# Performance work log

Hardware: AMD Instinct MI355X
Metric: run time of the kernel (lower is better)

The kernel has to match this reference:

```python
import jax, jax.numpy as jnp
import numpy as np
from jax import lax

IN_CH = 512
OUT_CH = 512
K = 3
W_DIM = 512
PAD = K // 2
EPS = 1e-8


def setup_inputs() -> dict:
    key = jax.random.key(0)
    k1, k2, k3, k4 = jax.random.split(key, 4)
    B, H, W = 8, 64, 64
    x = jax.random.normal(k1, (B, IN_CH, H, W), dtype=jnp.float32)
    w = jax.random.normal(k2, (B, W_DIM), dtype=jnp.float32)
    weight = jax.random.normal(k3, (OUT_CH, IN_CH, K, K), dtype=jnp.float32)
    bias = jnp.zeros((OUT_CH,), dtype=jnp.float32)
    # nn.Linear(512, in_ch): weight [in_ch, 512], bias [in_ch]
    lim = 1.0 / np.sqrt(W_DIM)
    affine_w = jax.random.uniform(k4, (IN_CH, W_DIM), dtype=jnp.float32, minval=-lim, maxval=lim)
    affine_b = jnp.zeros((IN_CH,), dtype=jnp.float32)
    return {"x": x, "w": w, "weight": weight, "bias": bias,
            "affine_w": affine_w, "affine_b": affine_b}


def _conv_one(xi, wi):
    # xi: [C, H, W], wi: [O, C, K, K] -> [O, H, W]
    out = lax.conv_general_dilated(
        xi[None], wi, window_strides=(1, 1),
        padding=[(PAD, PAD), (PAD, PAD)],
        dimension_numbers=("NCHW", "OIHW", "NCHW"))
    return out[0]


def reference(x, w, weight, bias, affine_w, affine_b):
    # style: [B, C] -> broadcast as [B, 1, C, 1, 1]
    style = w @ affine_w.T + affine_b
    wmod = weight[None] * (style[:, None, :, None, None] + 1.0)  # [B, O, C, K, K]
    # demodulate
    sigma = lax.rsqrt(jnp.sum(wmod * wmod, axis=(2, 3, 4), keepdims=True) + EPS)
    wmod = wmod * sigma
    # per-sample conv (equivalent to groups=B grouped conv)
    out = jax.vmap(_conv_one)(x, wmod)  # [B, O, H, W]
    return out + bias[None, :, None, None]
```

## Files before the change

kernel.cpp:

```cpp
#include <hip/hip_runtime.h>
#include <hip/hip_bf16.h>

typedef __attribute__((ext_vector_type(8))) short bf16x8;
typedef __attribute__((ext_vector_type(4))) float f32x4;

#define FSW(c) (((c) >> 1) & 3)

static __device__ __forceinline__ uint bf16rne(float f) {
    uint u = __float_as_uint(f);
    return (u + 0x7fffu + ((u >> 16) & 1u)) >> 16;
}

__global__ void k_prep1(const float* __restrict__ weight, ushort* __restrict__ Wf,
                        float* __restrict__ wsq, const float* __restrict__ w,
                        const float* __restrict__ aw, const float* __restrict__ ab,
                        float* __restrict__ style) {
    if (blockIdx.x < 1024) {
        int t = blockIdx.x * 256 + threadIdx.x;
        int o = t >> 9, c = t & 511;
        int grp = o >> 5, rr = o & 31, fm = rr >> 4, l15r = rr & 15;
        int chunkid = c >> 5, kgw = (c >> 3) & 3, kk = c & 7;
        int lanew = kgw * 16 + l15r;
        const float* wp = weight + (size_t)t * 9;
        size_t G = (size_t)(grp * 16 + chunkid);
        size_t base = G * 9216 + (size_t)fm * 512 + (size_t)lanew * 8 + kk;
        float sq = 0.f;
        #pragma unroll
        for (int j = 0; j < 9; ++j) {
            float v = wp[j];
            sq += v * v;
            Wf[base + (size_t)j * 1024] = (ushort)bf16rne(v);
        }
        wsq[t] = sq;
    } else {
        int idx = (blockIdx.x - 1024) * 4 + (threadIdx.x >> 6);
        int lane = threadIdx.x & 63;
        int b = idx >> 9, c = idx & 511;
        const float* wp = w + b * 512;
        const float* ap = aw + (size_t)c * 512;
        float s = 0.f;
        #pragma unroll
        for (int i = 0; i < 8; ++i) s += wp[lane + i * 64] * ap[lane + i * 64];
        #pragma unroll
        for (int m = 32; m; m >>= 1) s += __shfl_xor(s, m, 64);
        if (lane == 0) style[idx] = s + ab[c] + 1.0f;
    }
}

__global__ void k_prep2(const float* __restrict__ style, const float* __restrict__ wsq,
                        float* __restrict__ sigma, const float* __restrict__ x,
                        ushort* __restrict__ xb) {
    if (blockIdx.x < 1024) {
        int idx = blockIdx.x * 4 + (threadIdx.x >> 6);
        int lane = threadIdx.x & 63;
        int b = idx >> 9, o = idx & 511;
        const float* sp = style + b * 512;
        const float* qp = wsq + (size_t)o * 512;
        float s = 0.f;
        #pragma unroll
        for (int i = 0; i < 8; ++i) {
            float st = sp[lane + i * 64];
            s += st * st * qp[lane + i * 64];
        }
        #pragma unroll
        for (int m = 32; m; m >>= 1) s += __shfl_xor(s, m, 64);
        if (lane == 0) sigma[idx] = rsqrtf(s + 1e-8f);
    } else {
        int bid = blockIdx.x - 1024;
        int b = bid >> 6, y = bid & 63;
        int xcol = threadIdx.x >> 2, cg = threadIdx.x & 3;
        const float* sp = style + b * 512;
        #pragma unroll 1
        for (int cb = 0; cb < 16; ++cb) {
            int c0 = cb * 32 + cg * 8;
            float v[8];
            #pragma unroll
            for (int j = 0; j < 8; ++j)
                v[j] = x[((size_t)(b * 512 + c0 + j) * 64 + y) * 64 + xcol] * sp[c0 + j];
            uint4 pk;
            pk.x = bf16rne(v[0]) | (bf16rne(v[1]) << 16);
            pk.y = bf16rne(v[2]) | (bf16rne(v[3]) << 16);
            pk.z = bf16rne(v[4]) | (bf16rne(v[5]) << 16);
            pk.w = bf16rne(v[6]) | (bf16rne(v[7]) << 16);
            *(uint4*)&xb[((size_t)(b * 64 + y) * 64 + xcol) * 512 + c0] = pk;
        }
    }
}

#define ALOAD(SL, DY, CC) { \
    const ushort* p_ = Wbase + (size_t)(CC) * 9216 + (DY) * 3072; \
    _Pragma("unroll") for (int q_ = 0; q_ < 6; ++q_) \
        SL[q_] = *(const uint4*)(p_ + q_ * 512); }

#define MM(AV, BV, FM, FN) \
    acc[FM][FN] = __builtin_amdgcn_mfma_f32_16x16x32_bf16( \
        *(const bf16x8*)&(AV), (BV), acc[FM][FN], 0, 0, 0)

#define HGROUP(AARR, H) \
    _Pragma("unroll") for (int dx_ = 0; dx_ < 3; ++dx_) { \
      _Pragma("unroll") for (int q_ = 0; q_ < 4; ++q_) { \
        MM(AARR[dx_ * 2 + 0], bv[dx_ * 4 + q_], 0, (H) * 4 + q_); \
        MM(AARR[dx_ * 2 + 1], bv[dx_ * 4 + q_], 1, (H) * 4 + q_); \
      } }

#define ROW(R, MFMAS) { \
    bf16x8 bv[12]; \
    _Pragma("unroll") for (int dx_ = 0; dx_ < 3; ++dx_) \
    _Pragma("unroll") for (int q_ = 0; q_ < 4; ++q_) { \
        int ci_ = dx_ + q_ * 16 + l15; \
        bv[dx_ * 4 + q_] = *(const bf16x8*)&sX[cur][((R) * 66 + ci_) * 32 + ((kg ^ FSW(ci_)) * 8)]; \
    } \
    __builtin_amdgcn_s_setprio(1); \
    MFMAS \
    __builtin_amdgcn_s_setprio(0); }

__global__ __launch_bounds__(256, 2) void k_conv(
    const ushort* __restrict__ xb, const ushort* __restrict__ Wf,
    const float* __restrict__ sigma, const float* __restrict__ bias,
    float* __restrict__ out) {

    __shared__ ushort sX[2][4 * 66 * 32];

    const int tid = threadIdx.x, bid = blockIdx.x;
    const int ob = bid >> 8;
    const int pb = ((bid & 7) << 5) | ((bid >> 3) & 31);
    const int b = pb >> 5, y0 = (pb & 31) * 2;
    const int o0 = ob * 128;
    const int wv = tid >> 6, lane = tid & 63;
    const int l15 = lane & 15, kg = lane >> 4;

    const int scol = (tid >> 2) & 63;
    const int skg = tid & 3;
    const int colpos = scol + 1;
    const int sslot = (skg ^ FSW(colpos)) * 8;
    const ushort* xrow_base = xb + ((size_t)(b * 64) * 64 + scol) * 512 + skg * 8;

    const int grp = ob * 4 + wv;
    const ushort* Wbase = Wf + (size_t)grp * 147456 + lane * 8;

    f32x4 acc[2][8];
    #pragma unroll
    for (int i = 0; i < 2; ++i)
        #pragma unroll
        for (int j = 0; j < 8; ++j) acc[i][j] = (f32x4){0.f, 0.f, 0.f, 0.f};

    if (tid < 64) {
        int buf = tid >> 5, rem = tid & 31;
        int r = rem >> 3, side = (rem >> 2) & 1, sl = rem & 3;
        int cp = side * 65;
        *(uint4*)&sX[buf][(r * 66 + cp) * 32 + sl * 8] = make_uint4(0u, 0u, 0u, 0u);
    }

    uint4 xs[4];
    #pragma unroll
    for (int p = 0; p < 4; ++p) {
        int yy = y0 - 1 + p;
        xs[p] = ((unsigned)yy < 64u)
              ? *(const uint4*)(xrow_base + (size_t)yy * 32768)
              : make_uint4(0u, 0u, 0u, 0u);
    }
    #pragma unroll
    for (int p = 0; p < 4; ++p)
        *(uint4*)&sX[0][(p * 66 + colpos) * 32 + sslot] = xs[p];

    uint4 a0[6], a1[6], a2[6];
    ALOAD(a0, 0, 0) ALOAD(a1, 1, 0) ALOAD(a2, 2, 0)
    __syncthreads();

    int cur = 0;
    #pragma unroll 1
    for (int cci = 0; cci < 16; ++cci) {
        const int ncc = (cci + 1) & 15;

        #pragma unroll
        for (int p = 0; p < 4; ++p) {
            int yy = y0 - 1 + p;
            xs[p] = ((unsigned)yy < 64u)
                  ? *(const uint4*)(xrow_base + (size_t)yy * 32768 + ncc * 32)
                  : make_uint4(0u, 0u, 0u, 0u);
        }

        ROW(0, HGROUP(a0, 0))
        ROW(1, HGROUP(a0, 1) HGROUP(a1, 0))
        ALOAD(a0, 0, ncc)
        ROW(2, HGROUP(a1, 1) HGROUP(a2, 0))
        ALOAD(a1, 1, ncc)
        ROW(3, HGROUP(a2, 1))

        #pragma unroll
        for (int p = 0; p < 4; ++p)
            *(uint4*)&sX[cur ^ 1][(p * 66 + colpos) * 32 + sslot] = xs[p];
        __syncthreads();
        cur ^= 1;
        ALOAD(a2, 2, ncc)
    }

    const float* sigb = sigma + b * 512;
    #pragma unroll
    for (int fm = 0; fm < 2; ++fm) {
        #pragma unroll
        for (int j = 0; j < 4; ++j) {
            int o = o0 + wv * 32 + fm * 16 + kg * 4 + j;
            float sg = sigb[o];
            float bs = bias[o];
            float* op = out + ((size_t)(b * 512 + o) * 64 + y0) * 64;
            #pragma unroll
            for (int fn = 0; fn < 8; ++fn)
                op[(fn >> 2) * 64 + (fn & 3) * 16 + l15] = acc[fm][fn][j] * sg + bs;
        }
    }
}

extern "C" void kernel_launch(void* const* d_in, const int* in_sizes, int n_in,
                              void* d_out, int out_size, void* d_ws, size_t ws_size,
                              hipStream_t stream) {
    const float* x    = (const float*)d_in[0];
    const float* w    = (const float*)d_in[1];
    const float* wt   = (const float*)d_in[2];
    const float* bias = (const float*)d_in[3];
    const float* aw   = (const float*)d_in[4];
    const float* ab   = (const float*)d_in[5];
    float* out = (float*)d_out;

    float* style  = (float*)d_ws;
    float* sigmap = style + 4096;
    float* wsq    = sigmap + 4096;
    ushort* Wf    = (ushort*)(wsq + 512 * 512);
    ushort* xbm   = Wf + 2359296;

    k_prep1<<<2048, 256, 0, stream>>>(wt, Wf, wsq, w, aw, ab, style);
    k_prep2<<<1536, 256, 0, stream>>>(style, wsq, sigmap, x, xbm);
    k_conv <<<1024, 256, 0, stream>>>(xbm, Wf, sigmap, bias, out);
}
```

Before: 142.4 us.

## Process two channel chunks per barrier using four LDS planes, drop setprio

The conv main loop now handles two 32-channel chunks per iteration and stages input tiles in four LDS planes (two pairs) instead of two. This halves the number of __syncthreads barriers per block and keeps the weight register prefetch pipelined across both halves. The s_setprio hints around the MFMA groups are also removed. In exchange LDS use per block doubles (about 67 KB), which could limit occupancy to fewer than the two blocks per CU requested.

```diff
diff --git a/kernel.cpp b/kernel.cpp
--- a/kernel.cpp
+++ b/kernel.cpp
@@ -103,23 +103,33 @@
         MM(AARR[dx_ * 2 + 1], bv[dx_ * 4 + q_], 1, (H) * 4 + q_); \
       } }
 
-#define ROW(R, MFMAS) { \
+#define ROW(PL, R, MFMAS) { \
     bf16x8 bv[12]; \
     _Pragma("unroll") for (int dx_ = 0; dx_ < 3; ++dx_) \
     _Pragma("unroll") for (int q_ = 0; q_ < 4; ++q_) { \
         int ci_ = dx_ + q_ * 16 + l15; \
-        bv[dx_ * 4 + q_] = *(const bf16x8*)&sX[cur][((R) * 66 + ci_) * 32 + ((kg ^ FSW(ci_)) * 8)]; \
+        bv[dx_ * 4 + q_] = *(const bf16x8*)&(PL)[((R) * 66 + ci_) * 32 + ((kg ^ FSW(ci_)) * 8)]; \
     } \
-    __builtin_amdgcn_s_setprio(1); \
-    MFMAS \
-    __builtin_amdgcn_s_setprio(0); }
+    MFMAS }
+
+#define XLOAD(CC) { \
+    _Pragma("unroll") for (int p_ = 0; p_ < 4; ++p_) { \
+        int yy_ = y0 - 1 + p_; \
+        xs[p_] = ((unsigned)yy_ < 64u) \
+               ? *(const uint4*)(xrow_base + (size_t)yy_ * 32768 + (CC) * 32) \
+               : make_uint4(0u, 0u, 0u, 0u); \
+    } }
+
+#define XWRITE(PL) { \
+    _Pragma("unroll") for (int p_ = 0; p_ < 4; ++p_) \
+        *(uint4*)&(PL)[(p_ * 66 + colpos) * 32 + sslot] = xs[p_]; }
 
 __global__ __launch_bounds__(256, 2) void k_conv(
     const ushort* __restrict__ xb, const ushort* __restrict__ Wf,
     const float* __restrict__ sigma, const float* __restrict__ bias,
     float* __restrict__ out) {
 
-    __shared__ ushort sX[2][4 * 66 * 32];
+    __shared__ ushort sX[4][4 * 66 * 32];
 
     const int tid = threadIdx.x, bid = blockIdx.x;
     const int ob = bid >> 8;
@@ -144,24 +154,16 @@
         #pragma unroll
         for (int j = 0; j < 8; ++j) acc[i][j] = (f32x4){0.f, 0.f, 0.f, 0.f};
 
-    if (tid < 64) {
-        int buf = tid >> 5, rem = tid & 31;
+    if (tid < 128) {
+        int pl = tid >> 5, rem = tid & 31;
         int r = rem >> 3, side = (rem >> 2) & 1, sl = rem & 3;
         int cp = side * 65;
-        *(uint4*)&sX[buf][(r * 66 + cp) * 32 + sl * 8] = make_uint4(0u, 0u, 0u, 0u);
+        *(uint4*)&sX[pl][(r * 66 + cp) * 32 + sl * 8] = make_uint4(0u, 0u, 0u, 0u);
     }
 
     uint4 xs[4];
-    #pragma unroll
-    for (int p = 0; p < 4; ++p) {
-        int yy = y0 - 1 + p;
-        xs[p] = ((unsigned)yy < 64u)
-              ? *(const uint4*)(xrow_base + (size_t)yy * 32768)
-              : make_uint4(0u, 0u, 0u, 0u);
-    }
-    #pragma unroll
-    for (int p = 0; p < 4; ++p)
-        *(uint4*)&sX[0][(p * 66 + colpos) * 32 + sslot] = xs[p];
+    XLOAD(0) XWRITE(sX[0])
+    XLOAD(1) XWRITE(sX[1])
 
     uint4 a0[6], a1[6], a2[6];
     ALOAD(a0, 0, 0) ALOAD(a1, 1, 0) ALOAD(a2, 2, 0)
@@ -169,30 +171,33 @@
 
     int cur = 0;
     #pragma unroll 1
-    for (int cci = 0; cci < 16; ++cci) {
-        const int ncc = (cci + 1) & 15;
-
-        #pragma unroll
-        for (int p = 0; p < 4; ++p) {
-            int yy = y0 - 1 + p;
-            xs[p] = ((unsigned)yy < 64u)
-                  ? *(const uint4*)(xrow_base + (size_t)yy * 32768 + ncc * 32)
-                  : make_uint4(0u, 0u, 0u, 0u);
-        }
-
-        ROW(0, HGROUP(a0, 0))
-        ROW(1, HGROUP(a0, 1) HGROUP(a1, 0))
-        ALOAD(a0, 0, ncc)
-        ROW(2, HGROUP(a1, 1) HGROUP(a2, 0))
-        ALOAD(a1, 1, ncc)
-        ROW(3, HGROUP(a2, 1))
-
-        #pragma unroll
-        for (int p = 0; p < 4; ++p)
-            *(uint4*)&sX[cur ^ 1][(p * 66 + colpos) * 32 + sslot] = xs[p];
+    for (int it = 0; it < 8; ++it) {
+        const int c1 = it * 2 + 1;
+        const int n0 = (it * 2 + 2) & 15, n1 = (it * 2 + 3) & 15;
+        const int cur2 = cur * 2;
+
+        XLOAD(n0)
+        ROW(sX[cur2], 0, HGROUP(a0, 0))
+        ROW(sX[cur2], 1, HGROUP(a0, 1) HGROUP(a1, 0))
+        ALOAD(a0, 0, c1)
+        ROW(sX[cur2], 2, HGROUP(a1, 1) HGROUP(a2, 0))
+        ALOAD(a1, 1, c1)
+        ROW(sX[cur2], 3, HGROUP(a2, 1))
+        XWRITE(sX[cur2 ^ 2])
+
+        XLOAD(n1)
+        ALOAD(a2, 2, c1)
+        ROW(sX[cur2 + 1], 0, HGROUP(a0, 0))
+        ROW(sX[cur2 + 1], 1, HGROUP(a0, 1) HGROUP(a1, 0))
+        ALOAD(a0, 0, n0)
+        ROW(sX[cur2 + 1], 2, HGROUP(a1, 1) HGROUP(a2, 0))
+        ALOAD(a1, 1, n0)
+        ROW(sX[cur2 + 1], 3, HGROUP(a2, 1))
+        XWRITE(sX[(cur2 ^ 2) + 1])
+
         __syncthreads();
         cur ^= 1;
-        ALOAD(a2, 2, ncc)
+        ALOAD(a2, 2, n0)
     }
 
     const float* sigb = sigma + b * 512;
```

Measured after the change: 147.9 us. 1.04x slower.

## Retile conv waves to 2x2 layout with 64 out-channels by 32 columns

Applied to the files above, without the earlier changes.

Changes each wave's output tile from 32 out-channels by 64 pixels to 64 out-channels by 32 pixels, arranged as a 2x2 wave grid. Each wave now reads half as many shared-memory B fragments per row and twice as many A (weight) fragments from global memory. The A-register pipeline is reworked to ping-pong two 12-entry buffers across chunk pairs, with the loop unrolled by two. The aim is less LDS traffic per MFMA, at the cost of duplicated global weight loads across wave pairs and higher register pressure.

```diff
diff --git a/kernel.cpp b/kernel.cpp
--- a/kernel.cpp
+++ b/kernel.cpp
@@ -88,31 +88,55 @@
 }
 
 #define ALOAD(SL, DY, CC) { \
-    const ushort* p_ = Wbase + (size_t)(CC) * 9216 + (DY) * 3072; \
-    _Pragma("unroll") for (int q_ = 0; q_ < 6; ++q_) \
-        SL[q_] = *(const uint4*)(p_ + q_ * 512); }
-
-#define MM(AV, BV, FM, FN) \
-    acc[FM][FN] = __builtin_amdgcn_mfma_f32_16x16x32_bf16( \
-        *(const bf16x8*)&(AV), (BV), acc[FM][FN], 0, 0, 0)
+    _Pragma("unroll") for (int dx_ = 0; dx_ < 3; ++dx_) \
+    _Pragma("unroll") for (int fm_ = 0; fm_ < 4; ++fm_) \
+        SL[dx_ * 4 + fm_] = *(const uint4*)((fm_ < 2 ? Wbase0 : Wbase1) \
+            + (size_t)(CC) * 9216 + ((DY) * 3 + dx_) * 1024 + (fm_ & 1) * 512); }
 
 #define HGROUP(AARR, H) \
-    _Pragma("unroll") for (int dx_ = 0; dx_ < 3; ++dx_) { \
-      _Pragma("unroll") for (int q_ = 0; q_ < 4; ++q_) { \
-        MM(AARR[dx_ * 2 + 0], bv[dx_ * 4 + q_], 0, (H) * 4 + q_); \
-        MM(AARR[dx_ * 2 + 1], bv[dx_ * 4 + q_], 1, (H) * 4 + q_); \
-      } }
+    _Pragma("unroll") for (int dx_ = 0; dx_ < 3; ++dx_) \
+    _Pragma("unroll") for (int q_ = 0; q_ < 2; ++q_) \
+    _Pragma("unroll") for (int fm_ = 0; fm_ < 4; ++fm_) \
+        acc[fm_][(H) * 2 + q_] = __builtin_amdgcn_mfma_f32_16x16x32_bf16( \
+            *(const bf16x8*)&AARR[dx_ * 4 + fm_], bv[dx_ * 2 + q_], \
+            acc[fm_][(H) * 2 + q_], 0, 0, 0);
 
 #define ROW(R, MFMAS) { \
-    bf16x8 bv[12]; \
+    bf16x8 bv[6]; \
     _Pragma("unroll") for (int dx_ = 0; dx_ < 3; ++dx_) \
-    _Pragma("unroll") for (int q_ = 0; q_ < 4; ++q_) { \
-        int ci_ = dx_ + q_ * 16 + l15; \
-        bv[dx_ * 4 + q_] = *(const bf16x8*)&sX[cur][((R) * 66 + ci_) * 32 + ((kg ^ FSW(ci_)) * 8)]; \
+    _Pragma("unroll") for (int q_ = 0; q_ < 2; ++q_) { \
+        int ci_ = dx_ + cb32 + q_ * 16 + l15; \
+        bv[dx_ * 2 + q_] = *(const bf16x8*)&sX[cur][((R) * 66 + ci_) * 32 + ((kg ^ FSW(ci_)) * 8)]; \
     } \
     __builtin_amdgcn_s_setprio(1); \
     MFMAS \
     __builtin_amdgcn_s_setprio(0); }
+
+#define XLOAD(CC) { \
+    _Pragma("unroll") for (int p_ = 0; p_ < 4; ++p_) { \
+        int yy_ = y0 - 1 + p_; \
+        xs[p_] = ((unsigned)yy_ < 64u) \
+               ? *(const uint4*)(xrow_base + (size_t)yy_ * 32768 + (CC) * 32) \
+               : make_uint4(0u, 0u, 0u, 0u); \
+    } }
+
+#define XWRITE(BUF) { \
+    _Pragma("unroll") for (int p_ = 0; p_ < 4; ++p_) \
+        *(uint4*)&sX[BUF][(p_ * 66 + colpos) * 32 + sslot] = xs[p_]; }
+
+#define CHUNK(CCI, NCC, A0_, A1_) { \
+    XLOAD(NCC) \
+    ROW(0, HGROUP(A0_, 0)) \
+    ROW(1, HGROUP(A0_, 1) HGROUP(A1_, 0)) \
+    ALOAD(A0_, 2, CCI)             \
+    ROW(2, HGROUP(A1_, 1) HGROUP(A0_, 0)) \
+    ALOAD(A1_, 0, NCC)             \
+    ROW(3, HGROUP(A0_, 1)) \
+    XWRITE(cur ^ 1) \
+    __syncthreads(); \
+    cur ^= 1; \
+    ALOAD(A0_, 1, NCC)             \
+}
 
 __global__ __launch_bounds__(256, 2) void k_conv(
     const ushort* __restrict__ xb, const ushort* __restrict__ Wf,
@@ -128,6 +152,8 @@
     const int o0 = ob * 128;
     const int wv = tid >> 6, lane = tid & 63;
     const int l15 = lane & 15, kg = lane >> 4;
+    const int wr = wv >> 1;
+    const int cb32 = (wv & 1) * 32;
 
     const int scol = (tid >> 2) & 63;
     const int skg = tid & 3;
@@ -135,14 +161,14 @@
     const int sslot = (skg ^ FSW(colpos)) * 8;
     const ushort* xrow_base = xb + ((size_t)(b * 64) * 64 + scol) * 512 + skg * 8;
 
-    const int grp = ob * 4 + wv;
-    const ushort* Wbase = Wf + (size_t)grp * 147456 + lane * 8;
-
-    f32x4 acc[2][8];
+    const ushort* Wbase0 = Wf + (size_t)(ob * 4 + wr * 2) * 147456 + lane * 8;
+    const ushort* Wbase1 = Wbase0 + 147456;
+
+    f32x4 acc[4][4];
     #pragma unroll
-    for (int i = 0; i < 2; ++i)
-        #pragma unroll
-        for (int j = 0; j < 8; ++j) acc[i][j] = (f32x4){0.f, 0.f, 0.f, 0.f};
+    for (int i = 0; i < 4; ++i)
+        #pragma unroll
+        for (int j = 0; j < 4; ++j) acc[i][j] = (f32x4){0.f, 0.f, 0.f, 0.f};
 
     if (tid < 64) {
         int buf = tid >> 5, rem = tid & 31;
@@ -152,61 +178,35 @@
     }
 
     uint4 xs[4];
-    #pragma unroll
-    for (int p = 0; p < 4; ++p) {
-        int yy = y0 - 1 + p;
-        xs[p] = ((unsigned)yy < 64u)
-              ? *(const uint4*)(xrow_base + (size_t)yy * 32768)
-              : make_uint4(0u, 0u, 0u, 0u);
-    }
-    #pragma unroll
-    for (int p = 0; p < 4; ++p)
-        *(uint4*)&sX[0][(p * 66 + colpos) * 32 + sslot] = xs[p];
-
-    uint4 a0[6], a1[6], a2[6];
-    ALOAD(a0, 0, 0) ALOAD(a1, 1, 0) ALOAD(a2, 2, 0)
+    XLOAD(0)
+    XWRITE(0)
+
+    uint4 aX[12], aY[12];
+    ALOAD(aX, 0, 0) ALOAD(aY, 1, 0)
     __syncthreads();
 
     int cur = 0;
     #pragma unroll 1
-    for (int cci = 0; cci < 16; ++cci) {
-        const int ncc = (cci + 1) & 15;
-
-        #pragma unroll
-        for (int p = 0; p < 4; ++p) {
-            int yy = y0 - 1 + p;
-            xs[p] = ((unsigned)yy < 64u)
-                  ? *(const uint4*)(xrow_base + (size_t)yy * 32768 + ncc * 32)
-                  : make_uint4(0u, 0u, 0u, 0u);
-        }
-
-        ROW(0, HGROUP(a0, 0))
-        ROW(1, HGROUP(a0, 1) HGROUP(a1, 0))
-        ALOAD(a0, 0, ncc)
-        ROW(2, HGROUP(a1, 1) HGROUP(a2, 0))
-        ALOAD(a1, 1, ncc)
-        ROW(3, HGROUP(a2, 1))
-
-        #pragma unroll
-        for (int p = 0; p < 4; ++p)
-            *(uint4*)&sX[cur ^ 1][(p * 66 + colpos) * 32 + sslot] = xs[p];
-        __syncthreads();
-        cur ^= 1;
-        ALOAD(a2, 2, ncc)
+    for (int it = 0; it < 8; ++it) {
+        const int c0 = it * 2, c1 = it * 2 + 1, c2 = (it * 2 + 2) & 15;
+        CHUNK(c0, c1, aX, aY)
+        CHUNK(c1, c2, aY, aX)
     }
 
     const float* sigb = sigma + b * 512;
     #pragma unroll
-    for (int fm = 0; fm < 2; ++fm) {
+    for (int fm = 0; fm < 4; ++fm) {
         #pragma unroll
         for (int j = 0; j < 4; ++j) {
-            int o = o0 + wv * 32 + fm * 16 + kg * 4 + j;
+            int o = o0 + wr * 64 + fm * 16 + kg * 4 + j;
             float sg = sigb[o];
             float bs = bias[o];
             float* op = out + ((size_t)(b * 512 + o) * 64 + y0) * 64;
             #pragma unroll
-            for (int fn = 0; fn < 8; ++fn)
-                op[(fn >> 2) * 64 + (fn & 3) * 16 + l15] = acc[fm][fn][j] * sg + bs;
+            for (int h = 0; h < 2; ++h)
+                #pragma unroll
+                for (int q = 0; q < 2; ++q)
+                    op[h * 64 + cb32 + q * 16 + l15] = acc[fm][h * 2 + q][j] * sg + bs;
         }
     }
 }
```

Result: slower. 152.2 us (+6.9%).
